# Performance work log

Hardware: AMD Instinct MI355X
Metric: run time of the kernel (lower is better)

## Reference

```python
import jax, jax.numpy as jnp
import numpy as np

N = 8192        # num_nodes == args.input_size (code ties them together)
H = 64          # hidden_size
E = 262144      # num edges (avg degree 32)
FIN = N + H     # GCNConv in_channels = input_size + hidden_size


def _glorot(key, shape):
    fan_in, fan_out = shape
    lim = np.sqrt(6.0 / (fan_in + fan_out)).astype(np.float32)
    return jax.random.uniform(key, shape, jnp.float32, -lim, lim)


def gcn_conv(x, W, b, src, dst, n):
    """PyG GCNConv: lin -> add self-loops -> sym-normalized scatter-add -> +bias."""
    h = x @ W                                   # [n, out]
    loop = jnp.arange(n, dtype=src.dtype)
    s = jnp.concatenate([src, loop])            # [E+n]
    d = jnp.concatenate([dst, loop])
    deg = jax.ops.segment_sum(jnp.ones(s.shape[0], h.dtype), d, num_segments=n)
    dinv = jnp.where(deg > 0, jax.lax.rsqrt(deg), 0.0)
    norm = dinv[s] * dinv[d]                    # [E+n]
    out = jax.ops.segment_sum(h[s] * norm[:, None], d, num_segments=n)
    return out + b


def setup_inputs() -> dict:
    key = jax.random.key(0)
    k1, k2, k3, k4, k5 = jax.random.split(key, 5)
    x = jax.random.normal(k1, (N, N), jnp.float32)
    hidden_state = jax.random.normal(k2, (N, H), jnp.float32)
    W1 = _glorot(k3, (FIN, 2 * H))
    b1 = jnp.ones((2 * H,), jnp.float32)        # reset_parameters: constant_(bias, 1.0)
    W2 = _glorot(k4, (FIN, H))
    b2 = jnp.zeros((H,), jnp.float32)           # PyG default bias init = zeros
    edge_index = jax.random.randint(k5, (2, E), 0, N, jnp.int32)
    return {"x": x, "hidden_state": hidden_state, "W1": W1, "b1": b1,
            "W2": W2, "b2": b2, "edge_index": edge_index}


def reference(x, hidden_state, W1, b1, W2, b2, edge_index):
    src, dst = edge_index[0], edge_index[1]
    ru_input = jnp.concatenate([x, hidden_state], axis=1)        # [N, N+H]
    ru = jax.nn.sigmoid(gcn_conv(ru_input, W1, b1, src, dst, N))  # [N, 2H]
    flat = ru.reshape(-1, N * 2 * H)                              # [1, N*2H]
    r = flat[:, : N * H].reshape(-1, H)                           # [N, H]
    u = flat[:, N * H :].reshape(-1, H)                           # [N, H]
    c_input = jnp.concatenate([x, r * hidden_state], axis=1)
    c = jnp.tanh(gcn_conv(c_input, W2, b2, src, dst, N))          # [N, H]
    new_hidden_state = u * hidden_state + (1.0 - u) * c
    return new_hidden_state
```

## Files before the change

kernel.cpp:

```cpp
#include <hip/hip_runtime.h>
#include <hip/hip_bf16.h>
#include <stdint.h>

typedef __bf16 bf16x8 __attribute__((ext_vector_type(8)));
typedef float  f32x4  __attribute__((ext_vector_type(4)));
typedef unsigned uint4v __attribute__((ext_vector_type(4)));
using bf16 = __hip_bfloat16;

#define NNODES 8192
#define FIN    8256
#define NCOL   192
#define KT32   258
#define BMB    128

enum : size_t {
  WCT_OFF  = 0,
  CNT_OFF  = 3170304,
  OFF_OFF  = 3203072,
  CUR_OFF  = 3236096,
  DNV_OFF  = 3268864,
  CSR_OFF  = 3301632,
  H1_OFF   = 4350208,
  HX2_OFF  = 8544512,
  RU_OFF   = 10641664,
  H2_OFF   = 14835968,
  YP_OFF   = 16933120,
  YP_SLICE = 6291456
};

__global__ void k_zero_i(int* p, int n) {
  int i = blockIdx.x * 256 + threadIdx.x;
  if (i < n) p[i] = 0;
}

__global__ void k_out_zero(float* out) {
  int i = blockIdx.x * 256 + threadIdx.x;
  if (i < NNODES * 64) out[i] = 0.f;
}

__global__ void k_prep_wctf(const float* __restrict__ W1, const float* __restrict__ W2,
                            bf16* __restrict__ wctf) {
  int gid = blockIdx.x * 256 + threadIdx.x;
  if (gid >= KT32 * 12 * 64) return;
  int t = gid / 768;
  int rem = gid - t * 768;
  int nf = rem >> 6, lane = rem & 63;
  int col = nf * 16 + (lane & 15);
  int k0 = t * 32 + (lane >> 4) * 8;
  union { bf16 h[8]; uint4 v; } u;
#pragma unroll
  for (int j = 0; j < 8; ++j) {
    int k = k0 + j;
    float v;
    if (col < 128)      v = W1[(size_t)k * 128 + col];
    else if (k < 8192)  v = W2[(size_t)k * 64 + (col - 128)];
    else                v = 0.f;
    u.h[j] = __float2bfloat16(v);
  }
  *(uint4*)(wctf + (size_t)gid * 8) = u.v;
}

__global__ void k_hist(const int* __restrict__ ei, int E, int* cnt) {
  int e = blockIdx.x * 256 + threadIdx.x;
  if (e < E) atomicAdd(&cnt[ei[E + e]], 1);
}

__global__ void k_scan(const int* __restrict__ cnt, int* __restrict__ offs,
                       int* __restrict__ cur, float* __restrict__ dinv) {
  __shared__ int part[256];
  int tid = threadIdx.x;
  int base = tid * 32;
  int s = 0;
#pragma unroll
  for (int j = 0; j < 32; j++) s += cnt[base + j];
  part[tid] = s;
  __syncthreads();
  for (int off = 1; off < 256; off <<= 1) {
    int a = (tid >= off) ? part[tid - off] : 0;
    __syncthreads();
    part[tid] += a;
    __syncthreads();
  }
  int run = (tid == 0) ? 0 : part[tid - 1];
  for (int j = 0; j < 32; j++) {
    int c = cnt[base + j];
    offs[base + j] = run;
    cur[base + j]  = run;
    dinv[base + j] = rsqrtf((float)(c + 1));
    run += c;
  }
  if (tid == 255) offs[NNODES] = run;
}

__global__ void k_fill(const int* __restrict__ ei, int E, int* cur, int* __restrict__ csr) {
  int e = blockIdx.x * 256 + threadIdx.x;
  if (e < E) {
    int d = ei[E + e];
    int p = atomicAdd(&cur[d], 1);
    csr[p] = ei[e];
  }
}

__device__ __forceinline__ bf16x8 pack8(float4 a, float4 b) {
  union { bf16 h[8]; bf16x8 v; } u;
  u.h[0] = __float2bfloat16(a.x); u.h[1] = __float2bfloat16(a.y);
  u.h[2] = __float2bfloat16(a.z); u.h[3] = __float2bfloat16(a.w);
  u.h[4] = __float2bfloat16(b.x); u.h[5] = __float2bfloat16(b.y);
  u.h[6] = __float2bfloat16(b.z); u.h[7] = __float2bfloat16(b.w);
  return u.v;
}

union F4 { uint4v u; float4 f; bf16x8 h; };

__device__ __forceinline__ void gld16(void* ldsdst, const void* gsrc) {
  __builtin_amdgcn_global_load_lds(
      (__attribute__((address_space(1))) void*)gsrc,
      (__attribute__((address_space(3))) void*)ldsdst, 16, 0, 0);
}

__global__ __launch_bounds__(256, 2) void k_gemm(const float* __restrict__ x,
                                                 const float* __restrict__ hid,
                                                 const bf16* __restrict__ wctf,
                                                 float* __restrict__ yp,
                                                 bf16* __restrict__ h1d,
                                                 float* __restrict__ hx2d,
                                                 int tpc) {
  __shared__ __align__(1024) unsigned char smem[69632];
  const int tid = threadIdx.x;
  const int lane = tid & 63, w = tid >> 6;
  const int rl = lane & 15, g = lane >> 4;
  const int m0 = blockIdx.x * BMB;
  const int chunk = blockIdx.y;
  const int t_lo = chunk * tpc;
  const int t_hi = (t_lo + tpc > KT32) ? KT32 : (t_lo + tpc);
  const int nt = t_hi - t_lo;
  if (nt <= 0) return;

  const float* asx[4]; const float* ash[4];
#pragma unroll
  for (int q = 0; q < 4; ++q) {
    int u = q * 256 + tid, row = u >> 3, s = u & 7;
    int sel = (s ^ (row & 7)) << 2;
    asx[q] = x + (size_t)(m0 + row) * 8192 + sel;
    ash[q] = hid + (size_t)(m0 + row) * 64 + sel;
  }

#define STAGE_A(buf, t) do {                                                    \
    const int _t = (t);                                                         \
    unsigned _d = (unsigned)(buf) * 16384u;                                     \
    if (_t < 256) {                                                             \
      const int _k = _t * 32;                                                   \
      _Pragma("unroll")                                                         \
      for (int q = 0; q < 4; ++q)                                               \
        gld16(smem + _d + (unsigned)(q * 256 + tid) * 16u, asx[q] + _k);        \
    } else {                                                                    \
      const int _k = (_t - 256) * 32;                                           \
      _Pragma("unroll")                                                         \
      for (int q = 0; q < 4; ++q)                                               \
        gld16(smem + _d + (unsigned)(q * 256 + tid) * 16u, ash[q] + _k);        \
    }                                                                           \
  } while (0)

#define STAGE_B(buf, t) do {                                                    \
    const bf16* _bt = wctf + (size_t)(t) * 6144;                                \
    unsigned _d = 32768u + (unsigned)(buf) * 12288u;                            \
    _Pragma("unroll")                                                           \
    for (int q = 0; q < 3; ++q)                                                 \
      gld16(smem + _d + (unsigned)(q * 256 + tid) * 16u,                        \
            _bt + (size_t)(q * 256 + tid) * 8);                                 \
  } while (0)

  f32x4 acc0[12] = {};
  f32x4 acc1[12] = {};

  const unsigned sl0 = (unsigned)((g * 2) ^ (rl & 7));
  const unsigned sl1 = (unsigned)((g * 2 + 1) ^ (rl & 7));
  const unsigned ldsbase = (unsigned)(uintptr_t)&smem[0];
  const unsigned aA0 = (unsigned)(w * 32 + rl) * 128u + sl0 * 16u;
  const unsigned aA1 = (unsigned)(w * 32 + rl) * 128u + sl1 * 16u;
  const unsigned bB  = 32768u + (unsigned)lane * 16u;

  STAGE_A(0, t_lo);
  STAGE_B(0, t_lo);
  if (nt > 1) STAGE_B(1, t_lo + 1);

  int b3r = 0, b3w = 2;
  for (int i = 0; i < nt; ++i) {
    if (i + 2 < nt) STAGE_B(b3w, t_lo + i + 2);
    if (i + 1 < nt) STAGE_A((i + 1) & 1, t_lo + i + 1);

    if (i + 2 < nt)      asm volatile("s_waitcnt vmcnt(7)" ::: "memory");
    else if (i + 1 < nt) asm volatile("s_waitcnt vmcnt(4)" ::: "memory");
    else                 asm volatile("s_waitcnt vmcnt(0)" ::: "memory");
    asm volatile("s_barrier" ::: "memory");

    const unsigned ar = ldsbase + (unsigned)(i & 1) * 16384u;
    const unsigned br = ldsbase + bB + (unsigned)b3r * 12288u;
    F4 a00, a01, a10, a11, bv[12];
    asm volatile("ds_read_b128 %0, %1" : "=v"(a00.u) : "v"(ar + aA0));
    asm volatile("ds_read_b128 %0, %1" : "=v"(a01.u) : "v"(ar + aA1));
    asm volatile("ds_read_b128 %0, %1 offset:2048" : "=v"(a10.u) : "v"(ar + aA0));
    asm volatile("ds_read_b128 %0, %1 offset:2048" : "=v"(a11.u) : "v"(ar + aA1));
#pragma unroll
    for (int nf = 0; nf < 12; ++nf)
      asm volatile("ds_read_b128 %0, %1 offset:%c2"
                   : "=v"(bv[nf].u) : "v"(br), "i"(nf * 1024));
    asm volatile("s_waitcnt lgkmcnt(0)" ::: "memory");
    __builtin_amdgcn_sched_barrier(0);

    bf16x8 af0 = pack8(a00.f, a01.f);
    bf16x8 af1 = pack8(a10.f, a11.f);
#pragma unroll
    for (int nf = 0; nf < 12; ++nf) {
      acc0[nf] = __builtin_amdgcn_mfma_f32_16x16x32_bf16(af0, bv[nf].h, acc0[nf], 0, 0, 0);
      acc1[nf] = __builtin_amdgcn_mfma_f32_16x16x32_bf16(af1, bv[nf].h, acc1[nf], 0, 0, 0);
    }
    asm volatile("s_barrier" ::: "memory");
    b3r = (b3r == 2) ? 0 : b3r + 1;
    b3w = (b3w == 2) ? 0 : b3w + 1;
  }
#undef STAGE_A
#undef STAGE_B

  if (h1d) {
#pragma unroll
    for (int nf = 0; nf < 12; ++nf) {
      int col = nf * 16 + rl;
#pragma unroll
      for (int tt = 0; tt < 4; ++tt) {
        int ra = m0 + w * 32 + g * 4 + tt;
        int rb = ra + 16;
        if (col < 128) {
          h1d[(size_t)ra * 128 + col] = __float2bfloat16(acc0[nf][tt]);
          h1d[(size_t)rb * 128 + col] = __float2bfloat16(acc1[nf][tt]);
        } else {
          hx2d[(size_t)ra * 64 + (col - 128)] = acc0[nf][tt];
          hx2d[(size_t)rb * 64 + (col - 128)] = acc1[nf][tt];
        }
      }
    }
  } else {
    float* ypc = yp + (size_t)chunk * ((size_t)NNODES * NCOL);
#pragma unroll
    for (int nf = 0; nf < 12; ++nf) {
      int col = nf * 16 + rl;
#pragma unroll
      for (int tt = 0; tt < 4; ++tt) {
        int ra = m0 + w * 32 + g * 4 + tt;
        ypc[(size_t)ra * NCOL + col] = acc0[nf][tt];
        ypc[(size_t)(ra + 16) * NCOL + col] = acc1[nf][tt];
      }
    }
  }
}

__global__ void k_reduce4(const float* __restrict__ yp, bf16* __restrict__ h1,
                          float* __restrict__ hx2, int nch) {
  int u = blockIdx.x * 256 + threadIdx.x;
  float4 s = {0.f, 0.f, 0.f, 0.f};
  for (int c = 0; c < nch; c++) {
    float4 v = *(const float4*)(yp + (size_t)c * ((size_t)NNODES * NCOL) + (size_t)u * 4);
    s.x += v.x; s.y += v.y; s.z += v.z; s.w += v.w;
  }
  int e = u * 4;
  int i = e / NCOL, c = e - i * NCOL;
  if (c < 128) {
    bf16* dst = h1 + (size_t)i * 128 + c;
    dst[0] = __float2bfloat16(s.x); dst[1] = __float2bfloat16(s.y);
    dst[2] = __float2bfloat16(s.z); dst[3] = __float2bfloat16(s.w);
  } else {
    *(float4*)(hx2 + (size_t)i * 64 + (c - 128)) = s;
  }
}

__device__ __forceinline__ float bflo(unsigned v) { return __uint_as_float(v << 16); }
__device__ __forceinline__ float bfhi(unsigned v) { return __uint_as_float(v & 0xffff0000u); }

__global__ void k_scat1(const bf16* __restrict__ h1b, const int* __restrict__ offs,
                        const int* __restrict__ csr, const float* __restrict__ dinv,
                        const float* __restrict__ b1, float* __restrict__ ru) {
  int node = blockIdx.x * 4 + (threadIdx.x >> 6);
  int lane = threadIdx.x & 63;
  const unsigned* h1u = (const unsigned*)h1b;
  float dd = dinv[node];
  unsigned vv = h1u[(size_t)node * 64 + lane];
  float ax = bflo(vv) * dd * dd, ay = bfhi(vv) * dd * dd;
  int e0 = offs[node], e1 = offs[node + 1];
  for (int e = e0; e < e1; ++e) {
    int s = csr[e];
    float nrm = dinv[s] * dd;
    unsigned wv = h1u[(size_t)s * 64 + lane];
    ax += bflo(wv) * nrm;
    ay += bfhi(wv) * nrm;
  }
  ax += b1[lane * 2];
  ay += b1[lane * 2 + 1];
  ax = 1.f / (1.f + expf(-ax));
  ay = 1.f / (1.f + expf(-ay));
  ru[(size_t)node * 128 + lane * 2]     = ax;
  ru[(size_t)node * 128 + lane * 2 + 1] = ay;
}

__global__ void k_rh(const float* __restrict__ ru, const float* __restrict__ hidden,
                     const float* __restrict__ hx2, const float* __restrict__ W2,
                     bf16* __restrict__ h2) {
  __shared__ float W2s[64][64];
  __shared__ float rhs[4][64];
  int tid = threadIdx.x;
#pragma unroll
  for (int t = 0; t < 16; ++t) {
    int idx = tid + 256 * t;
    int j = idx >> 6, c = idx & 63;
    W2s[j][c] = W2[(size_t)(8192 + j) * 64 + c];
  }
  int w = tid >> 6, lane = tid & 63;
  int i = blockIdx.x * 4 + w;
  float rv = ru[(size_t)(i >> 1) * 128 + ((i & 1) << 6) + lane];
  float hv = hidden[(size_t)i * 64 + lane];
  rhs[w][lane] = rv * hv;
  __syncthreads();
  float acc = hx2[(size_t)i * 64 + lane];
#pragma unroll 8
  for (int j = 0; j < 64; ++j) acc += rhs[w][j] * W2s[j][lane];
  h2[(size_t)i * 64 + lane] = __float2bfloat16(acc);
}

__global__ void k_scat2(const bf16* __restrict__ h2b, const int* __restrict__ offs,
                        const int* __restrict__ csr, const float* __restrict__ dinv,
                        const float* __restrict__ b2, const float* __restrict__ ru,
                        const float* __restrict__ hidden, float* __restrict__ out) {
  int node = blockIdx.x * 4 + (threadIdx.x >> 6);
  int lane = threadIdx.x & 63;
  const unsigned short* h2u = (const unsigned short*)h2b;
  float dd = dinv[node];
  float acc = bflo((unsigned)h2u[(size_t)node * 64 + lane]) * dd * dd;
  int e0 = offs[node], e1 = offs[node + 1];
  for (int e = e0; e < e1; ++e) {
    int s = csr[e];
    acc += bflo((unsigned)h2u[(size_t)s * 64 + lane]) * dinv[s] * dd;
  }
  acc += b2[lane];
  float cv = tanhf(acc);
  float u = ru[(size_t)(4096 + (node >> 1)) * 128 + ((node & 1) << 6) + lane];
  float hv = hidden[(size_t)node * 64 + lane];
  out[(size_t)node * 64 + lane] = u * hv + (1.f - u) * cv;
}

extern "C" void kernel_launch(void* const* d_in, const int* in_sizes, int n_in,
                              void* d_out, int out_size, void* d_ws, size_t ws_size,
                              hipStream_t stream) {
  (void)n_in; (void)out_size;
  const float* x   = (const float*)d_in[0];
  const float* hid = (const float*)d_in[1];
  const float* W1  = (const float*)d_in[2];
  const float* b1  = (const float*)d_in[3];
  const float* W2  = (const float*)d_in[4];
  const float* b2  = (const float*)d_in[5];
  const int*   ei  = (const int*)d_in[6];
  const int E = in_sizes[6] / 2;
  float* out = (float*)d_out;

  int ksplit;
  if      (ws_size >= YP_OFF + 8ull * YP_SLICE) ksplit = 8;
  else if (ws_size >= YP_OFF + 4ull * YP_SLICE) ksplit = 4;
  else if (ws_size >= YP_OFF + 2ull * YP_SLICE) ksplit = 2;
  else if (ws_size >= YP_OFF)                   ksplit = 1;
  else {
    k_out_zero<<<dim3(NNODES * 64 / 256), dim3(256), 0, stream>>>(out);
    return;
  }
  const int tpc = (KT32 + ksplit - 1) / ksplit;

  char* ws = (char*)d_ws;
  bf16*  wctf = (bf16*)(ws + WCT_OFF);
  int*   cnt  = (int*)(ws + CNT_OFF);
  int*   offs = (int*)(ws + OFF_OFF);
  int*   cur  = (int*)(ws + CUR_OFF);
  float* dinv = (float*)(ws + DNV_OFF);
  int*   csr  = (int*)(ws + CSR_OFF);
  bf16*  h1   = (bf16*)(ws + H1_OFF);
  float* hx2  = (float*)(ws + HX2_OFF);
  float* ru   = (float*)(ws + RU_OFF);
  bf16*  h2   = (bf16*)(ws + H2_OFF);
  float* yp   = (float*)(ws + YP_OFF);

  k_zero_i<<<dim3(32), dim3(256), 0, stream>>>(cnt, NNODES);
  k_prep_wctf<<<dim3((KT32 * 12 * 64 + 255) / 256), dim3(256), 0, stream>>>(W1, W2, wctf);
  k_hist<<<dim3((E + 255) / 256), dim3(256), 0, stream>>>(ei, E, cnt);
  k_scan<<<dim3(1), dim3(256), 0, stream>>>(cnt, offs, cur, dinv);
  k_fill<<<dim3((E + 255) / 256), dim3(256), 0, stream>>>(ei, E, cur, csr);
  if (ksplit == 1) {
    k_gemm<<<dim3(NNODES / BMB, 1), dim3(256), 0, stream>>>(x, hid, wctf, nullptr, h1, hx2, tpc);
  } else {
    k_gemm<<<dim3(NNODES / BMB, ksplit), dim3(256), 0, stream>>>(x, hid, wctf, yp, nullptr, nullptr, tpc);
    k_reduce4<<<dim3(NNODES * NCOL / 1024), dim3(256), 0, stream>>>(yp, h1, hx2, ksplit);
  }
  k_scat1<<<dim3(NNODES / 4), dim3(256), 0, stream>>>(h1, offs, csr, dinv, b1, ru);
  k_rh<<<dim3(NNODES / 4), dim3(256), 0, stream>>>(ru, hid, hx2, W2, h2);
  k_scat2<<<dim3(NNODES / 4), dim3(256), 0, stream>>>(h2, offs, csr, dinv, b2, ru, hid, out);
}
```

Measured before the change: 207.5 us.

## Load A operand directly from global into registers, bypassing LDS staging

The fp32 A tile (x / hidden rows) is no longer staged through LDS with global_load_lds. Each lane now issues its own global_load_dwordx4 into ping-pong register sets, and the loop is unrolled by two to alternate those sets. This shrinks LDS from 68KB to 36KB and removes the A-side ds_reads, which could raise occupancy. In exchange there are more VGPRs for the prefetch registers and less coalesced global access, since each lane reads 32 bytes from a separate row. The vmcnt waits keep their old counts, which still match because four A loads and three B loads are in flight.

Measured after the change: 209.4 us. Within noise of the previous version (+0.9%).

```diff
diff --git a/kernel.cpp b/kernel.cpp
--- a/kernel.cpp
+++ b/kernel.cpp
@@ -125,101 +125,94 @@
                                                  bf16* __restrict__ h1d,
                                                  float* __restrict__ hx2d,
                                                  int tpc) {
-  __shared__ __align__(1024) unsigned char smem[69632];
+  __shared__ __align__(1024) unsigned char smem[36864];
   const int tid = threadIdx.x;
   const int lane = tid & 63, w = tid >> 6;
   const int rl = lane & 15, g = lane >> 4;
   const int m0 = blockIdx.x * BMB;
+  const int r0 = m0 + w * 32 + rl, r1 = r0 + 16;
   const int chunk = blockIdx.y;
   const int t_lo = chunk * tpc;
   const int t_hi = (t_lo + tpc > KT32) ? KT32 : (t_lo + tpc);
   const int nt = t_hi - t_lo;
   if (nt <= 0) return;
 
-  const float* asx[4]; const float* ash[4];
-#pragma unroll
-  for (int q = 0; q < 4; ++q) {
-    int u = q * 256 + tid, row = u >> 3, s = u & 7;
-    int sel = (s ^ (row & 7)) << 2;
-    asx[q] = x + (size_t)(m0 + row) * 8192 + sel;
-    ash[q] = hid + (size_t)(m0 + row) * 64 + sel;
-  }
-
-#define STAGE_A(buf, t) do {                                                    \
-    const int _t = (t);                                                         \
-    unsigned _d = (unsigned)(buf) * 16384u;                                     \
-    if (_t < 256) {                                                             \
-      const int _k = _t * 32;                                                   \
-      _Pragma("unroll")                                                         \
-      for (int q = 0; q < 4; ++q)                                               \
-        gld16(smem + _d + (unsigned)(q * 256 + tid) * 16u, asx[q] + _k);        \
-    } else {                                                                    \
-      const int _k = (_t - 256) * 32;                                           \
-      _Pragma("unroll")                                                         \
-      for (int q = 0; q < 4; ++q)                                               \
-        gld16(smem + _d + (unsigned)(q * 256 + tid) * 16u, ash[q] + _k);        \
-    }                                                                           \
-  } while (0)
+  const float* a0x = x + (size_t)r0 * 8192 + g * 8;
+  const float* a1x = x + (size_t)r1 * 8192 + g * 8;
+  const float* a0h = hid + (size_t)r0 * 64 + g * 8;
+  const float* a1h = hid + (size_t)r1 * 64 + g * 8;
 
 #define STAGE_B(buf, t) do {                                                    \
     const bf16* _bt = wctf + (size_t)(t) * 6144;                                \
-    unsigned _d = 32768u + (unsigned)(buf) * 12288u;                            \
+    unsigned _d = (unsigned)(buf) * 12288u;                                     \
     _Pragma("unroll")                                                           \
     for (int q = 0; q < 3; ++q)                                                 \
       gld16(smem + _d + (unsigned)(q * 256 + tid) * 16u,                        \
             _bt + (size_t)(q * 256 + tid) * 8);                                 \
   } while (0)
 
+#define LOAD_A(Pa, Pb, Pc, Pd, T) do {                                          \
+    const int _k = (T) * 32;                                                    \
+    const float* _p0 = (_k < 8192) ? (a0x + _k) : (a0h + (_k - 8192));          \
+    const float* _p1 = (_k < 8192) ? (a1x + _k) : (a1h + (_k - 8192));          \
+    asm volatile("global_load_dwordx4 %0, %1, off"           : "=v"(Pa.u) : "v"(_p0)); \
+    asm volatile("global_load_dwordx4 %0, %1, off offset:16" : "=v"(Pb.u) : "v"(_p0)); \
+    asm volatile("global_load_dwordx4 %0, %1, off"           : "=v"(Pc.u) : "v"(_p1)); \
+    asm volatile("global_load_dwordx4 %0, %1, off offset:16" : "=v"(Pd.u) : "v"(_p1)); \
+  } while (0)
+
   f32x4 acc0[12] = {};
   f32x4 acc1[12] = {};
-
-  const unsigned sl0 = (unsigned)((g * 2) ^ (rl & 7));
-  const unsigned sl1 = (unsigned)((g * 2 + 1) ^ (rl & 7));
+  F4 p00, p01, p10, p11, q00, q01, q10, q11;
+
   const unsigned ldsbase = (unsigned)(uintptr_t)&smem[0];
-  const unsigned aA0 = (unsigned)(w * 32 + rl) * 128u + sl0 * 16u;
-  const unsigned aA1 = (unsigned)(w * 32 + rl) * 128u + sl1 * 16u;
-  const unsigned bB  = 32768u + (unsigned)lane * 16u;
-
-  STAGE_A(0, t_lo);
+  const unsigned bB = (unsigned)lane * 16u;
+
   STAGE_B(0, t_lo);
   if (nt > 1) STAGE_B(1, t_lo + 1);
+  LOAD_A(p00, p01, p10, p11, t_lo);
 
   int b3r = 0, b3w = 2;
-  for (int i = 0; i < nt; ++i) {
-    if (i + 2 < nt) STAGE_B(b3w, t_lo + i + 2);
-    if (i + 1 < nt) STAGE_A((i + 1) & 1, t_lo + i + 1);
-
-    if (i + 2 < nt)      asm volatile("s_waitcnt vmcnt(7)" ::: "memory");
-    else if (i + 1 < nt) asm volatile("s_waitcnt vmcnt(4)" ::: "memory");
-    else                 asm volatile("s_waitcnt vmcnt(0)" ::: "memory");
-    asm volatile("s_barrier" ::: "memory");
-
-    const unsigned ar = ldsbase + (unsigned)(i & 1) * 16384u;
-    const unsigned br = ldsbase + bB + (unsigned)b3r * 12288u;
-    F4 a00, a01, a10, a11, bv[12];
-    asm volatile("ds_read_b128 %0, %1" : "=v"(a00.u) : "v"(ar + aA0));
-    asm volatile("ds_read_b128 %0, %1" : "=v"(a01.u) : "v"(ar + aA1));
-    asm volatile("ds_read_b128 %0, %1 offset:2048" : "=v"(a10.u) : "v"(ar + aA0));
-    asm volatile("ds_read_b128 %0, %1 offset:2048" : "=v"(a11.u) : "v"(ar + aA1));
-#pragma unroll
-    for (int nf = 0; nf < 12; ++nf)
-      asm volatile("ds_read_b128 %0, %1 offset:%c2"
-                   : "=v"(bv[nf].u) : "v"(br), "i"(nf * 1024));
-    asm volatile("s_waitcnt lgkmcnt(0)" ::: "memory");
-    __builtin_amdgcn_sched_barrier(0);
-
-    bf16x8 af0 = pack8(a00.f, a01.f);
-    bf16x8 af1 = pack8(a10.f, a11.f);
-#pragma unroll
-    for (int nf = 0; nf < 12; ++nf) {
-      acc0[nf] = __builtin_amdgcn_mfma_f32_16x16x32_bf16(af0, bv[nf].h, acc0[nf], 0, 0, 0);
-      acc1[nf] = __builtin_amdgcn_mfma_f32_16x16x32_bf16(af1, bv[nf].h, acc1[nf], 0, 0, 0);
-    }
-    asm volatile("s_barrier" ::: "memory");
-    b3r = (b3r == 2) ? 0 : b3r + 1;
-    b3w = (b3w == 2) ? 0 : b3w + 1;
-  }
-#undef STAGE_A
+
+#define GBODY(Ca, Cb, Cc, Cd, Na, Nb, Nc, Nd, I) do {                           \
+    const int _i = (I);                                                         \
+    if (_i + 2 < nt) STAGE_B(b3w, t_lo + _i + 2);                    \
+    if (_i + 1 < nt) LOAD_A(Na, Nb, Nc, Nd, t_lo + _i + 1);          \
+        \
+    if (_i + 2 < nt)      asm volatile("s_waitcnt vmcnt(7)" ::: "memory");      \
+    else if (_i + 1 < nt) asm volatile("s_waitcnt vmcnt(4)" ::: "memory");      \
+    else                  asm volatile("s_waitcnt vmcnt(0)" ::: "memory");      \
+    asm volatile("s_barrier" ::: "memory");         \
+    {                                                                           \
+      const unsigned _br = ldsbase + bB + (unsigned)b3r * 12288u;               \
+      F4 _bv[12];                                                               \
+      _Pragma("unroll")                                                         \
+      for (int nf = 0; nf < 12; ++nf)                                           \
+        asm volatile("ds_read_b128 %0, %1 offset:%c2"                           \
+                     : "=v"(_bv[nf].u) : "v"(_br), "i"(nf * 1024));             \
+      asm volatile("s_waitcnt lgkmcnt(0)" ::: "memory");                        \
+      __builtin_amdgcn_sched_barrier(0);                                        \
+      bf16x8 _af0 = pack8(Ca.f, Cb.f);                                          \
+      bf16x8 _af1 = pack8(Cc.f, Cd.f);                                          \
+      _Pragma("unroll")                                                         \
+      for (int nf = 0; nf < 12; ++nf) {                                         \
+        acc0[nf] = __builtin_amdgcn_mfma_f32_16x16x32_bf16(_af0, _bv[nf].h, acc0[nf], 0, 0, 0); \
+        acc1[nf] = __builtin_amdgcn_mfma_f32_16x16x32_bf16(_af1, _bv[nf].h, acc1[nf], 0, 0, 0); \
+      }                                                                         \
+    }                                                                           \
+    asm volatile("s_barrier" ::: "memory");   \
+    b3r = (b3r == 2) ? 0 : b3r + 1;                                             \
+    b3w = (b3w == 2) ? 0 : b3w + 1;                                             \
+  } while (0)
+
+  int it = 0;
+  for (; it + 1 < nt; it += 2) {
+    GBODY(p00, p01, p10, p11, q00, q01, q10, q11, it);
+    GBODY(q00, q01, q10, q11, p00, p01, p10, p11, it + 1);
+  }
+  if (it < nt) GBODY(p00, p01, p10, p11, q00, q01, q10, q11, it);
+#undef GBODY
+#undef LOAD_A
 #undef STAGE_B
 
   if (h1d) {
```
